# Performance work log

Measured on AMD Instinct MI355X. Metric: run time of the kernel, lower is better.

Reference implementation:

```python
import jax, jax.numpy as jnp
import numpy as np

NOISE_DIM = 128
IN_FEATURES = 512
OUT_FEATURES = 512
BATCH = 256


def setup_inputs() -> dict:
    key = jax.random.key(0)
    k1, k2, k3 = jax.random.split(key, 3)
    out_dim = IN_FEATURES * OUT_FEATURES + OUT_FEATURES
    # x = [noise | features]
    x = jax.random.normal(k1, (BATCH, NOISE_DIM + IN_FEATURES), dtype=jnp.float32)
    # hypermodel Linear params; scale ~ 1/sqrt(fan_in) like torch default init
    scale = 1.0 / np.sqrt(NOISE_DIM)
    W = jax.random.uniform(k2, (NOISE_DIM, out_dim), dtype=jnp.float32, minval=-scale, maxval=scale)
    b = jax.random.uniform(k3, (out_dim,), dtype=jnp.float32, minval=-scale, maxval=scale)
    return {"x": x, "W": W, "b": b}


def reference(x, W, b):
    # split input into hypernet noise and features
    noise = x[:, :NOISE_DIM]            # [B, noise_dim]
    feats = x[:, NOISE_DIM:]            # [B, in_features]
    # hypermodel: generate per-sample linear params
    params = noise @ W + b              # [B, in*out + out]
    w_flat = params[:, : IN_FEATURES * OUT_FEATURES]
    bias = params[:, IN_FEATURES * OUT_FEATURES :]        # [B, out]
    weight = w_flat.reshape(-1, IN_FEATURES, OUT_FEATURES)  # [B, in, out]
    # batched matmul (torch.bmm of [B,1,in] @ [B,in,out]) + bias, squeeze
    out = jnp.einsum("bi,bio->bo", feats, weight) + bias   # [B, out]
    return out
```

## Files before the change

kernel.cpp:

```cpp
#include <hip/hip_runtime.h>
#include <hip/hip_bf16.h>
#include <stdint.h>

namespace {
constexpr int kBatch = 256;
constexpr int kNoise = 128;
constexpr int kIn    = 512;
constexpr int kOut   = 512;
constexpr int kXCols = kNoise + kIn;
constexpr int kPCols = kIn * kOut + kOut;
constexpr int kOTile = 32;
constexpr int kITile = 16;
constexpr int kSplits = kIn / kITile;
constexpr int kWStride = 68;
constexpr int kFeatsStride = 260;
}

typedef __bf16 bf16x8 __attribute__((ext_vector_type(8)));
typedef float  f32x4  __attribute__((ext_vector_type(4)));
typedef unsigned int u32x4 __attribute__((ext_vector_type(4)));

__device__ inline unsigned int pack_bf16x2(float lo, float hi) {
    unsigned int a = (unsigned int)__builtin_bit_cast(unsigned short, (__bf16)lo);
    unsigned int b = (unsigned int)__builtin_bit_cast(unsigned short, (__bf16)hi);
    return a | (b << 16);
}

__device__ inline void wg_barrier_lds() {
    __asm__ volatile("" ::: "memory");
    __builtin_amdgcn_s_waitcnt(0xC07F);
    __builtin_amdgcn_s_barrier();
    __asm__ volatile("" ::: "memory");
}

__global__ __launch_bounds__(512, 4)
void hyper_gemm_kernel(const float* __restrict__ x,
                       const float* __restrict__ W,
                       const float* __restrict__ bvec,
                       float* __restrict__ part)
{
    const int tid  = threadIdx.x;
    const int lane = tid & 63;
    const int wave = tid >> 6;
    const int q    = lane >> 4;
    const int l16  = lane & 15;

    const int o0 = blockIdx.x * kOTile;
    const int i0 = blockIdx.y * kITile;

    const int u    = tid >> 3;
    const int colg = (tid & 7) * 4;

    __shared__ unsigned int wtile[2][kOTile * kWStride];
    __shared__ float feats_lds[kITile * kFeatsStride];
    __shared__ float bv_lds[(kITile + 1) * kOTile];

    const int nPass = (blockIdx.y == 0) ? (kITile + 1) : kITile;

    auto pass_cbase = [&](int p) -> size_t {
        return (p == kITile) ? (size_t)(kIn * kOut) : (size_t)(i0 + p) * kOut;
    };
    auto wrow = [&](int p) -> const float* {
        return W + (size_t)(2 * u) * kPCols + pass_cbase(p) + o0 + colg;
    };

    f32x4 pa0, pa1, pb0, pb1;
    { const float* wp = wrow(0); pa0 = *(const f32x4*)wp; pa1 = *(const f32x4*)(wp + kPCols); }
    { const float* wp = wrow(1); pb0 = *(const f32x4*)wp; pb1 = *(const f32x4*)(wp + kPCols); }

    for (int idx = tid; idx < (kITile + 1) * kOTile; idx += 512) {
        const int p = idx >> 5, c = idx & 31;
        const size_t cb = (p == kITile) ? (size_t)(kIn * kOut) : (size_t)(i0 + p) * kOut;
        bv_lds[idx] = bvec[cb + o0 + c];
    }

    {
        const int i    = tid & 15;
        const int brow = tid >> 4;
        #pragma unroll
        for (int rep = 0; rep < 8; ++rep) {
            const int b = brow + rep * 32;
            feats_lds[i * kFeatsStride + b] = x[b * kXCols + kNoise + i0 + i];
        }
    }

    bf16x8 afrag[2][4];
    {
        #pragma unroll
        for (int mt = 0; mt < 2; ++mt) {
            const float* xr = x + (size_t)(wave * 32 + mt * 16 + l16) * kXCols;
            #pragma unroll
            for (int s = 0; s < 4; ++s) {
                const float* p = xr + s * 32 + q * 8;
                f32x4 u0 = *(const f32x4*)(p);
                f32x4 u1 = *(const f32x4*)(p + 4);
                bf16x8 a;
                a[0] = (__bf16)u0[0]; a[1] = (__bf16)u0[1];
                a[2] = (__bf16)u0[2]; a[3] = (__bf16)u0[3];
                a[4] = (__bf16)u1[0]; a[5] = (__bf16)u1[1];
                a[6] = (__bf16)u1[2]; a[7] = (__bf16)u1[3];
                afrag[mt][s] = a;
            }
        }
    }

    float oacc[2][2][4];
    #pragma unroll
    for (int mt = 0; mt < 2; ++mt)
        #pragma unroll
        for (int nt = 0; nt < 2; ++nt)
            #pragma unroll
            for (int r = 0; r < 4; ++r) oacc[mt][nt][r] = 0.f;

    __syncthreads();

    for (int ip = 0; ip < nPass; ++ip) {
        unsigned int pk[4];
        #pragma unroll
        for (int cc = 0; cc < 4; ++cc) pk[cc] = pack_bf16x2(pa0[cc], pa1[cc]);

        unsigned int* wt = &wtile[ip & 1][0];
        #pragma unroll
        for (int cc = 0; cc < 4; ++cc)
            wt[(colg + cc) * kWStride + u] = pk[cc];

        pa0 = pb0; pa1 = pb1;
        if (ip + 2 < nPass) {
            const float* wp = wrow(ip + 2);
            pb0 = *(const f32x4*)wp; pb1 = *(const f32x4*)(wp + kPCols);
        }

        wg_barrier_lds();

        f32x4 acc[2][2];
        const f32x4 zero = {0.f, 0.f, 0.f, 0.f};
        #pragma unroll
        for (int mt = 0; mt < 2; ++mt)
            #pragma unroll
            for (int nt = 0; nt < 2; ++nt) acc[mt][nt] = zero;

        #pragma unroll
        for (int s = 0; s < 4; ++s) {
            #pragma unroll
            for (int nt = 0; nt < 2; ++nt) {
                u32x4 raw = *(const u32x4*)&wt[(nt * 16 + l16) * kWStride + s * 16 + q * 4];
                bf16x8 bfrag = __builtin_bit_cast(bf16x8, raw);
                #pragma unroll
                for (int mt = 0; mt < 2; ++mt)
                    acc[mt][nt] = __builtin_amdgcn_mfma_f32_16x16x32_bf16(
                        afrag[mt][s], bfrag, acc[mt][nt], 0, 0, 0);
            }
        }

        const float bv0 = bv_lds[ip * kOTile + l16];
        const float bv1 = bv_lds[ip * kOTile + 16 + l16];

        if (ip < kITile) {
            #pragma unroll
            for (int mt = 0; mt < 2; ++mt) {
                const f32x4 f4 = *(const f32x4*)&feats_lds[ip * kFeatsStride
                                        + wave * 32 + mt * 16 + q * 4];
                #pragma unroll
                for (int r = 0; r < 4; ++r) {
                    oacc[mt][0][r] += f4[r] * (acc[mt][0][r] + bv0);
                    oacc[mt][1][r] += f4[r] * (acc[mt][1][r] + bv1);
                }
            }
        } else {
            #pragma unroll
            for (int mt = 0; mt < 2; ++mt)
                #pragma unroll
                for (int r = 0; r < 4; ++r) {
                    oacc[mt][0][r] += acc[mt][0][r] + bv0;
                    oacc[mt][1][r] += acc[mt][1][r] + bv1;
                }
        }
    }

    float* pp = part + (size_t)blockIdx.y * kBatch * kOut;
    #pragma unroll
    for (int mt = 0; mt < 2; ++mt)
        #pragma unroll
        for (int nt = 0; nt < 2; ++nt) {
            const int o = o0 + nt * 16 + l16;
            #pragma unroll
            for (int r = 0; r < 4; ++r) {
                const int b = wave * 32 + mt * 16 + q * 4 + r;
                pp[(size_t)b * kOut + o] = oacc[mt][nt][r];
            }
        }
}

__global__ __launch_bounds__(256)
void reduce_kernel(const float* __restrict__ part, float* __restrict__ out)
{
    const size_t idx4 = ((size_t)blockIdx.x * 256 + threadIdx.x) * 4;
    f32x4 acc = *(const f32x4*)(part + idx4);
    #pragma unroll
    for (int s = 1; s < kSplits; ++s)
        acc += *(const f32x4*)(part + (size_t)s * kBatch * kOut + idx4);
    *(f32x4*)(out + idx4) = acc;
}

extern "C" void kernel_launch(void* const* d_in, const int* in_sizes, int n_in,
                              void* d_out, int out_size, void* d_ws, size_t ws_size,
                              hipStream_t stream) {
    const float* x  = (const float*)d_in[0];
    const float* W  = (const float*)d_in[1];
    const float* bv = (const float*)d_in[2];
    float* out  = (float*)d_out;
    float* part = (float*)d_ws;

    dim3 grid(kOut / kOTile, kSplits);
    hyper_gemm_kernel<<<grid, 512, 0, stream>>>(x, W, bv, part);

    const int n4 = kBatch * kOut / 4;
    reduce_kernel<<<n4 / 256, 256, 0, stream>>>(part, out);
}
```

Measured before the change: 217.6 us.

## Refactor contraction to fold features into noise operand, split noise dim with atomics

The GEMM is reorganized so each pass multiplies (feature times noise) as the A operand against a bf16 tile of W, and the results accumulate directly in MFMA accumulators across input rows. This avoids the separate per-pass epilogue. The noise dimension is split across a third grid axis, with atomicAdd into zeroed partial slabs via a memset. The bias-vector and W-bias contributions become extra MFMA passes, with the final bias added in the reduce. Output tiles widen to 128 columns with a swizzled LDS layout, which adds atomic traffic and a memset launch in exchange for more parallelism and higher MFMA utilization.

```diff
diff --git a/kernel.cpp b/kernel.cpp
--- a/kernel.cpp
+++ b/kernel.cpp
@@ -9,11 +9,13 @@
 constexpr int kOut   = 512;
 constexpr int kXCols = kNoise + kIn;
 constexpr int kPCols = kIn * kOut + kOut;
-constexpr int kOTile = 32;
-constexpr int kITile = 16;
-constexpr int kSplits = kIn / kITile;
-constexpr int kWStride = 68;
+constexpr int kWBias = kIn * kOut;
+constexpr int kOTileC = 128;
+constexpr int kITile  = 16;
+constexpr int kNChunk = 32;
+constexpr int kWTStride = 20;
 constexpr int kFeatsStride = 260;
+constexpr int kSlabs = 32;
 }
 
 typedef __bf16 bf16x8 __attribute__((ext_vector_type(8)));
@@ -32,6 +34,8 @@
     __builtin_amdgcn_s_barrier();
     __asm__ volatile("" ::: "memory");
 }
+
+struct PInfo { const float* p; int stride; int rowlim; };
 
 __global__ __launch_bounds__(512, 4)
 void hyper_gemm_kernel(const float* __restrict__ x,
@@ -45,34 +49,52 @@
     const int q    = lane >> 4;
     const int l16  = lane & 15;
 
-    const int o0 = blockIdx.x * kOTile;
-    const int i0 = blockIdx.y * kITile;
-
-    const int u    = tid >> 3;
-    const int colg = (tid & 7) * 4;
-
-    __shared__ unsigned int wtile[2][kOTile * kWStride];
+    const int obk = blockIdx.x;
+    const int isp = blockIdx.y;
+    const int nc  = blockIdx.z;
+    const int o0  = obk * kOTileC;
+    const int i0  = isp * kITile;
+    const int n0  = nc  * kNChunk;
+
+    const bool hasBv = (nc == 0);
+    const bool hasWb = (isp == 0);
+    const int nPass = kITile + (hasBv ? 1 : 0) + (hasWb ? 1 : 0);
+
+    const int rp = tid >> 5;
+    const int w  = tid & 31;
+    const int wkey = w & 3;
+    const int rkey = (l16 >> 2) & 3;
+
+    __shared__ unsigned int wtile[2][kOTileC * kWTStride];
     __shared__ float feats_lds[kITile * kFeatsStride];
-    __shared__ float bv_lds[(kITile + 1) * kOTile];
-
-    const int nPass = (blockIdx.y == 0) ? (kITile + 1) : kITile;
-
-    auto pass_cbase = [&](int p) -> size_t {
-        return (p == kITile) ? (size_t)(kIn * kOut) : (size_t)(i0 + p) * kOut;
+
+    auto ptype = [&](int p) -> int {
+        if (p < kITile) return 0;
+        if (p == kITile) return hasBv ? 1 : 2;
+        return 2;
     };
-    auto wrow = [&](int p) -> const float* {
-        return W + (size_t)(2 * u) * kPCols + pass_cbase(p) + o0 + colg;
+    auto pinfo = [&](int p) -> PInfo {
+        const int t = ptype(p);
+        if (t == 0) return { W + (size_t)n0 * kPCols + (size_t)(i0 + p) * kOut + o0, kPCols, 32 };
+        if (t == 1) return { bvec + (size_t)i0 * kOut + o0, kOut, kITile };
+        return { W + (size_t)n0 * kPCols + kWBias + o0, kPCols, 32 };
     };
-
-    f32x4 pa0, pa1, pb0, pb1;
-    { const float* wp = wrow(0); pa0 = *(const f32x4*)wp; pa1 = *(const f32x4*)(wp + kPCols); }
-    { const float* wp = wrow(1); pb0 = *(const f32x4*)wp; pb1 = *(const f32x4*)(wp + kPCols); }
-
-    for (int idx = tid; idx < (kITile + 1) * kOTile; idx += 512) {
-        const int p = idx >> 5, c = idx & 31;
-        const size_t cb = (p == kITile) ? (size_t)(kIn * kOut) : (size_t)(i0 + p) * kOut;
-        bv_lds[idx] = bvec[cb + o0 + c];
-    }
+    auto load_pass = [&](int p, f32x4& lo, f32x4& hi) {
+        const PInfo pi = pinfo(p);
+        const int r = 2 * rp;
+        if (r < pi.rowlim) {
+            const float* base = pi.p + (size_t)r * pi.stride + 4 * w;
+            lo = *(const f32x4*)base;
+            hi = *(const f32x4*)(base + pi.stride);
+        } else {
+            lo = f32x4{0.f, 0.f, 0.f, 0.f};
+            hi = f32x4{0.f, 0.f, 0.f, 0.f};
+        }
+    };
+
+    f32x4 pla0, pla1, plb0, plb1;
+    load_pass(0, pla0, pla1);
+    load_pass(1, plb0, plb1);
 
     {
         const int i    = tid & 15;
@@ -80,124 +102,117 @@
         #pragma unroll
         for (int rep = 0; rep < 8; ++rep) {
             const int b = brow + rep * 32;
-            feats_lds[i * kFeatsStride + b] = x[b * kXCols + kNoise + i0 + i];
-        }
-    }
-
-    bf16x8 afrag[2][4];
-    {
-        #pragma unroll
-        for (int mt = 0; mt < 2; ++mt) {
-            const float* xr = x + (size_t)(wave * 32 + mt * 16 + l16) * kXCols;
-            #pragma unroll
-            for (int s = 0; s < 4; ++s) {
-                const float* p = xr + s * 32 + q * 8;
-                f32x4 u0 = *(const f32x4*)(p);
-                f32x4 u1 = *(const f32x4*)(p + 4);
-                bf16x8 a;
-                a[0] = (__bf16)u0[0]; a[1] = (__bf16)u0[1];
-                a[2] = (__bf16)u0[2]; a[3] = (__bf16)u0[3];
-                a[4] = (__bf16)u1[0]; a[5] = (__bf16)u1[1];
-                a[6] = (__bf16)u1[2]; a[7] = (__bf16)u1[3];
-                afrag[mt][s] = a;
-            }
-        }
-    }
-
-    float oacc[2][2][4];
-    #pragma unroll
-    for (int mt = 0; mt < 2; ++mt)
-        #pragma unroll
-        for (int nt = 0; nt < 2; ++nt)
-            #pragma unroll
-            for (int r = 0; r < 4; ++r) oacc[mt][nt][r] = 0.f;
+            feats_lds[i * kFeatsStride + b] = x[(size_t)b * kXCols + kNoise + i0 + i];
+        }
+    }
+
+    f32x4 nz[2][2];
+    #pragma unroll
+    for (int m = 0; m < 2; ++m) {
+        const float* xr = x + (size_t)((wave * 2 + m) * 16 + l16) * kXCols + n0 + q * 8;
+        nz[m][0] = *(const f32x4*)xr;
+        nz[m][1] = *(const f32x4*)(xr + 4);
+    }
+
+    f32x4 oacc[2][8];
+    #pragma unroll
+    for (int m = 0; m < 2; ++m)
+        #pragma unroll
+        for (int fo = 0; fo < 8; ++fo) oacc[m][fo] = f32x4{0.f, 0.f, 0.f, 0.f};
 
     __syncthreads();
 
     for (int ip = 0; ip < nPass; ++ip) {
         unsigned int pk[4];
         #pragma unroll
-        for (int cc = 0; cc < 4; ++cc) pk[cc] = pack_bf16x2(pa0[cc], pa1[cc]);
+        for (int cc = 0; cc < 4; ++cc) pk[cc] = pack_bf16x2(pla0[cc], pla1[cc]);
 
         unsigned int* wt = &wtile[ip & 1][0];
         #pragma unroll
         for (int cc = 0; cc < 4; ++cc)
-            wt[(colg + cc) * kWStride + u] = pk[cc];
-
-        pa0 = pb0; pa1 = pb1;
-        if (ip + 2 < nPass) {
-            const float* wp = wrow(ip + 2);
-            pb0 = *(const f32x4*)wp; pb1 = *(const f32x4*)(wp + kPCols);
-        }
+            wt[(4 * w + cc) * kWTStride + ((((rp >> 2) ^ wkey) << 2) | (rp & 3))] = pk[cc];
+
+        pla0 = plb0; pla1 = plb1;
+        if (ip + 2 < nPass) load_pass(ip + 2, plb0, plb1);
 
         wg_barrier_lds();
 
-        f32x4 acc[2][2];
-        const f32x4 zero = {0.f, 0.f, 0.f, 0.f};
-        #pragma unroll
-        for (int mt = 0; mt < 2; ++mt)
-            #pragma unroll
-            for (int nt = 0; nt < 2; ++nt) acc[mt][nt] = zero;
-
-        #pragma unroll
-        for (int s = 0; s < 4; ++s) {
-            #pragma unroll
-            for (int nt = 0; nt < 2; ++nt) {
-                u32x4 raw = *(const u32x4*)&wt[(nt * 16 + l16) * kWStride + s * 16 + q * 4];
-                bf16x8 bfrag = __builtin_bit_cast(bf16x8, raw);
+        const int t = ptype(ip);
+        bf16x8 afr[2];
+        if (t == 0) {
+            #pragma unroll
+            for (int m = 0; m < 2; ++m) {
+                const float f = feats_lds[ip * kFeatsStride + (wave * 2 + m) * 16 + l16];
+                bf16x8 a;
                 #pragma unroll
-                for (int mt = 0; mt < 2; ++mt)
-                    acc[mt][nt] = __builtin_amdgcn_mfma_f32_16x16x32_bf16(
-                        afrag[mt][s], bfrag, acc[mt][nt], 0, 0, 0);
+                for (int j = 0; j < 4; ++j) {
+                    a[j]     = (__bf16)(f * nz[m][0][j]);
+                    a[j + 4] = (__bf16)(f * nz[m][1][j]);
+                }
+                afr[m] = a;
             }
-        }
-
-        const float bv0 = bv_lds[ip * kOTile + l16];
-        const float bv1 = bv_lds[ip * kOTile + 16 + l16];
-
-        if (ip < kITile) {
-            #pragma unroll
-            for (int mt = 0; mt < 2; ++mt) {
-                const f32x4 f4 = *(const f32x4*)&feats_lds[ip * kFeatsStride
-                                        + wave * 32 + mt * 16 + q * 4];
+        } else if (t == 2) {
+            #pragma unroll
+            for (int m = 0; m < 2; ++m) {
+                bf16x8 a;
                 #pragma unroll
-                for (int r = 0; r < 4; ++r) {
-                    oacc[mt][0][r] += f4[r] * (acc[mt][0][r] + bv0);
-                    oacc[mt][1][r] += f4[r] * (acc[mt][1][r] + bv1);
+                for (int j = 0; j < 4; ++j) {
+                    a[j]     = (__bf16)nz[m][0][j];
+                    a[j + 4] = (__bf16)nz[m][1][j];
                 }
+                afr[m] = a;
             }
         } else {
             #pragma unroll
-            for (int mt = 0; mt < 2; ++mt)
+            for (int m = 0; m < 2; ++m) {
+                const int b = (wave * 2 + m) * 16 + l16;
+                bf16x8 a;
                 #pragma unroll
-                for (int r = 0; r < 4; ++r) {
-                    oacc[mt][0][r] += acc[mt][0][r] + bv0;
-                    oacc[mt][1][r] += acc[mt][1][r] + bv1;
+                for (int j = 0; j < 8; ++j) {
+                    const int kk = q * 8 + j;
+                    const float v = feats_lds[(kk & 15) * kFeatsStride + b];
+                    a[j] = (kk < kITile) ? (__bf16)v : (__bf16)0.f;
                 }
-        }
-    }
-
-    float* pp = part + (size_t)blockIdx.y * kBatch * kOut;
-    #pragma unroll
-    for (int mt = 0; mt < 2; ++mt)
-        #pragma unroll
-        for (int nt = 0; nt < 2; ++nt) {
-            const int o = o0 + nt * 16 + l16;
-            #pragma unroll
-            for (int r = 0; r < 4; ++r) {
-                const int b = wave * 32 + mt * 16 + q * 4 + r;
-                pp[(size_t)b * kOut + o] = oacc[mt][nt][r];
+                afr[m] = a;
             }
         }
+
+        #pragma unroll
+        for (int fo = 0; fo < 8; ++fo) {
+            const int col = fo * 16 + l16;
+            u32x4 raw = *(const u32x4*)&wt[col * kWTStride + ((q ^ rkey) << 2)];
+            bf16x8 bfr = __builtin_bit_cast(bf16x8, raw);
+            #pragma unroll
+            for (int m = 0; m < 2; ++m)
+                oacc[m][fo] = __builtin_amdgcn_mfma_f32_16x16x32_bf16(
+                    afr[m], bfr, oacc[m][fo], 0, 0, 0);
+        }
+    }
+
+    float* pp = part + (size_t)isp * (kBatch * kOut);
+    #pragma unroll
+    for (int m = 0; m < 2; ++m) {
+        const int bb = (wave * 2 + m) * 16 + q * 4;
+        #pragma unroll
+        for (int fo = 0; fo < 8; ++fo) {
+            const int o = o0 + fo * 16 + l16;
+            #pragma unroll
+            for (int r = 0; r < 4; ++r)
+                atomicAdd(&pp[(size_t)(bb + r) * kOut + o], oacc[m][fo][r]);
+        }
+    }
 }
 
 __global__ __launch_bounds__(256)
-void reduce_kernel(const float* __restrict__ part, float* __restrict__ out)
+void reduce_kernel(const float* __restrict__ part,
+                   const float* __restrict__ bvec,
+                   float* __restrict__ out)
 {
     const size_t idx4 = ((size_t)blockIdx.x * 256 + threadIdx.x) * 4;
-    f32x4 acc = *(const f32x4*)(part + idx4);
-    #pragma unroll
-    for (int s = 1; s < kSplits; ++s)
+    const int o = (int)(idx4 & (kOut - 1));
+    f32x4 acc = *(const f32x4*)(bvec + kWBias + o);
+    #pragma unroll
+    for (int s = 0; s < kSlabs; ++s)
         acc += *(const f32x4*)(part + (size_t)s * kBatch * kOut + idx4);
     *(f32x4*)(out + idx4) = acc;
 }
@@ -211,9 +226,11 @@
     float* out  = (float*)d_out;
     float* part = (float*)d_ws;
 
-    dim3 grid(kOut / kOTile, kSplits);
+    hipMemsetAsync(part, 0, (size_t)kSlabs * kBatch * kOut * sizeof(float), stream);
+
+    dim3 grid(kOut / kOTileC, kIn / kITile, kNoise / kNChunk);
     hyper_gemm_kernel<<<grid, 512, 0, stream>>>(x, W, bv, part);
 
     const int n4 = kBatch * kOut / 4;
-    reduce_kernel<<<n4 / 256, 256, 0, stream>>>(part, out);
-}
+    reduce_kernel<<<n4 / 256, 256, 0, stream>>>(part, bv, out);
+}
```

Result: slower. 261.2 us (+20.1%).

## Restructure W loads to per-column scalar gathers with register ring and peeled bias pass

Applied to the files above, without the earlier changes.

Each thread now loads one output column across 8 consecutive noise rows as scalar loads (coalesced 32-wide per row) instead of 4-wide vectors over 2 rows, then packs them into a single 128-bit LDS store. The main loop is fully unrolled over the fixed 16 passes, and the bias-generating pass for split 0 is peeled out of the loop, with its weights preloaded up front. Occupancy hint drops from 4 to 2 blocks to allow more registers for the unrolled loop and ring buffer. This targets the per-pass branching and the strided LDS transpose writes, at the cost of more global load instructions and possibly lower occupancy.

```diff
diff --git a/kernel.cpp b/kernel.cpp
--- a/kernel.cpp
+++ b/kernel.cpp
@@ -9,11 +9,13 @@
 constexpr int kOut   = 512;
 constexpr int kXCols = kNoise + kIn;
 constexpr int kPCols = kIn * kOut + kOut;
+constexpr int kWBias = kIn * kOut;
 constexpr int kOTile = 32;
 constexpr int kITile = 16;
 constexpr int kSplits = kIn / kITile;
 constexpr int kWStride = 68;
 constexpr int kFeatsStride = 260;
+constexpr int kDepth = 2;
 }
 
 typedef __bf16 bf16x8 __attribute__((ext_vector_type(8)));
@@ -33,7 +35,7 @@
     __asm__ volatile("" ::: "memory");
 }
 
-__global__ __launch_bounds__(512, 4)
+__global__ __launch_bounds__(512, 2)
 void hyper_gemm_kernel(const float* __restrict__ x,
                        const float* __restrict__ W,
                        const float* __restrict__ bvec,
@@ -48,29 +50,40 @@
     const int o0 = blockIdx.x * kOTile;
     const int i0 = blockIdx.y * kITile;
 
-    const int u    = tid >> 3;
-    const int colg = (tid & 7) * 4;
+    const int col = tid & 31;
+    const int kpp = tid >> 5;
 
     __shared__ unsigned int wtile[2][kOTile * kWStride];
     __shared__ float feats_lds[kITile * kFeatsStride];
     __shared__ float bv_lds[(kITile + 1) * kOTile];
 
-    const int nPass = (blockIdx.y == 0) ? (kITile + 1) : kITile;
-
-    auto pass_cbase = [&](int p) -> size_t {
-        return (p == kITile) ? (size_t)(kIn * kOut) : (size_t)(i0 + p) * kOut;
+    const bool hasWb = (blockIdx.y == 0);
+
+    auto wbase = [&](int p) -> const float* {
+        return W + (size_t)(8 * kpp) * kPCols + (size_t)(i0 + p) * kOut + o0 + col;
     };
-    auto wrow = [&](int p) -> const float* {
-        return W + (size_t)(2 * u) * kPCols + pass_cbase(p) + o0 + colg;
-    };
-
-    f32x4 pa0, pa1, pb0, pb1;
-    { const float* wp = wrow(0); pa0 = *(const f32x4*)wp; pa1 = *(const f32x4*)(wp + kPCols); }
-    { const float* wp = wrow(1); pb0 = *(const f32x4*)wp; pb1 = *(const f32x4*)(wp + kPCols); }
+
+    float wb[8];
+    #pragma unroll
+    for (int e = 0; e < 8; ++e) wb[e] = 0.f;
+    if (hasWb) {
+        const float* bp = W + (size_t)(8 * kpp) * kPCols + kWBias + o0 + col;
+        #pragma unroll
+        for (int e = 0; e < 8; ++e) wb[e] = bp[(size_t)e * kPCols];
+    }
+
+    float ring[kDepth][8];
+    #pragma unroll
+    for (int p = 0; p < kDepth; ++p) {
+        const float* wp = wbase(p);
+        #pragma unroll
+        for (int e = 0; e < 8; ++e)
+            ring[p][e] = wp[(size_t)e * kPCols];
+    }
 
     for (int idx = tid; idx < (kITile + 1) * kOTile; idx += 512) {
         const int p = idx >> 5, c = idx & 31;
-        const size_t cb = (p == kITile) ? (size_t)(kIn * kOut) : (size_t)(i0 + p) * kOut;
+        const size_t cb = (p == kITile) ? (size_t)kWBias : (size_t)(i0 + p) * kOut;
         bv_lds[idx] = bvec[cb + o0 + c];
     }
 
@@ -80,27 +93,25 @@
         #pragma unroll
         for (int rep = 0; rep < 8; ++rep) {
             const int b = brow + rep * 32;
-            feats_lds[i * kFeatsStride + b] = x[b * kXCols + kNoise + i0 + i];
+            feats_lds[i * kFeatsStride + b] = x[(size_t)b * kXCols + kNoise + i0 + i];
         }
     }
 
     bf16x8 afrag[2][4];
-    {
-        #pragma unroll
-        for (int mt = 0; mt < 2; ++mt) {
-            const float* xr = x + (size_t)(wave * 32 + mt * 16 + l16) * kXCols;
-            #pragma unroll
-            for (int s = 0; s < 4; ++s) {
-                const float* p = xr + s * 32 + q * 8;
-                f32x4 u0 = *(const f32x4*)(p);
-                f32x4 u1 = *(const f32x4*)(p + 4);
-                bf16x8 a;
-                a[0] = (__bf16)u0[0]; a[1] = (__bf16)u0[1];
-                a[2] = (__bf16)u0[2]; a[3] = (__bf16)u0[3];
-                a[4] = (__bf16)u1[0]; a[5] = (__bf16)u1[1];
-                a[6] = (__bf16)u1[2]; a[7] = (__bf16)u1[3];
-                afrag[mt][s] = a;
-            }
+    #pragma unroll
+    for (int mt = 0; mt < 2; ++mt) {
+        const float* xr = x + (size_t)(wave * 32 + mt * 16 + l16) * kXCols;
+        #pragma unroll
+        for (int s = 0; s < 4; ++s) {
+            const float* p = xr + s * 32 + q * 8;
+            f32x4 u0 = *(const f32x4*)(p);
+            f32x4 u1 = *(const f32x4*)(p + 4);
+            bf16x8 a;
+            a[0] = (__bf16)u0[0]; a[1] = (__bf16)u0[1];
+            a[2] = (__bf16)u0[2]; a[3] = (__bf16)u0[3];
+            a[4] = (__bf16)u1[0]; a[5] = (__bf16)u1[1];
+            a[6] = (__bf16)u1[2]; a[7] = (__bf16)u1[3];
+            afrag[mt][s] = a;
         }
     }
 
@@ -114,67 +125,104 @@
 
     __syncthreads();
 
-    for (int ip = 0; ip < nPass; ++ip) {
-        unsigned int pk[4];
-        #pragma unroll
-        for (int cc = 0; cc < 4; ++cc) pk[cc] = pack_bf16x2(pa0[cc], pa1[cc]);
+    #pragma unroll
+    for (int ip = 0; ip < kITile; ++ip) {
+        const int slot = ip & (kDepth - 1);
+
+        u32x4 pk;
+        pk[0] = pack_bf16x2(ring[slot][0], ring[slot][1]);
+        pk[1] = pack_bf16x2(ring[slot][2], ring[slot][3]);
+        pk[2] = pack_bf16x2(ring[slot][4], ring[slot][5]);
+        pk[3] = pack_bf16x2(ring[slot][6], ring[slot][7]);
 
         unsigned int* wt = &wtile[ip & 1][0];
-        #pragma unroll
-        for (int cc = 0; cc < 4; ++cc)
-            wt[(colg + cc) * kWStride + u] = pk[cc];
-
-        pa0 = pb0; pa1 = pb1;
-        if (ip + 2 < nPass) {
-            const float* wp = wrow(ip + 2);
-            pb0 = *(const f32x4*)wp; pb1 = *(const f32x4*)(wp + kPCols);
+        *(u32x4*)&wt[col * kWStride + 4 * kpp] = pk;
+
+        if (ip + kDepth < kITile) {
+            const float* wp = wbase(ip + kDepth);
+            #pragma unroll
+            for (int e = 0; e < 8; ++e)
+                ring[slot][e] = wp[(size_t)e * kPCols];
         }
 
         wg_barrier_lds();
 
         f32x4 acc[2][2];
-        const f32x4 zero = {0.f, 0.f, 0.f, 0.f};
         #pragma unroll
         for (int mt = 0; mt < 2; ++mt)
             #pragma unroll
-            for (int nt = 0; nt < 2; ++nt) acc[mt][nt] = zero;
+            for (int nt = 0; nt < 2; ++nt) acc[mt][nt] = f32x4{0.f, 0.f, 0.f, 0.f};
 
         #pragma unroll
         for (int s = 0; s < 4; ++s) {
+            bf16x8 bfr[2];
             #pragma unroll
             for (int nt = 0; nt < 2; ++nt) {
                 u32x4 raw = *(const u32x4*)&wt[(nt * 16 + l16) * kWStride + s * 16 + q * 4];
-                bf16x8 bfrag = __builtin_bit_cast(bf16x8, raw);
+                bfr[nt] = __builtin_bit_cast(bf16x8, raw);
+            }
+            #pragma unroll
+            for (int mt = 0; mt < 2; ++mt)
                 #pragma unroll
-                for (int mt = 0; mt < 2; ++mt)
+                for (int nt = 0; nt < 2; ++nt)
                     acc[mt][nt] = __builtin_amdgcn_mfma_f32_16x16x32_bf16(
-                        afrag[mt][s], bfrag, acc[mt][nt], 0, 0, 0);
-            }
+                        afrag[mt][s], bfr[nt], acc[mt][nt], 0, 0, 0);
         }
 
         const float bv0 = bv_lds[ip * kOTile + l16];
         const float bv1 = bv_lds[ip * kOTile + 16 + l16];
-
-        if (ip < kITile) {
-            #pragma unroll
-            for (int mt = 0; mt < 2; ++mt) {
-                const f32x4 f4 = *(const f32x4*)&feats_lds[ip * kFeatsStride
-                                        + wave * 32 + mt * 16 + q * 4];
-                #pragma unroll
-                for (int r = 0; r < 4; ++r) {
-                    oacc[mt][0][r] += f4[r] * (acc[mt][0][r] + bv0);
-                    oacc[mt][1][r] += f4[r] * (acc[mt][1][r] + bv1);
-                }
-            }
-        } else {
+        #pragma unroll
+        for (int mt = 0; mt < 2; ++mt) {
+            const f32x4 f4 = *(const f32x4*)&feats_lds[ip * kFeatsStride
+                                    + wave * 32 + mt * 16 + q * 4];
+            #pragma unroll
+            for (int r = 0; r < 4; ++r) {
+                oacc[mt][0][r] += f4[r] * (acc[mt][0][r] + bv0);
+                oacc[mt][1][r] += f4[r] * (acc[mt][1][r] + bv1);
+            }
+        }
+    }
+
+    if (hasWb) {
+        u32x4 pk;
+        pk[0] = pack_bf16x2(wb[0], wb[1]);
+        pk[1] = pack_bf16x2(wb[2], wb[3]);
+        pk[2] = pack_bf16x2(wb[4], wb[5]);
+        pk[3] = pack_bf16x2(wb[6], wb[7]);
+        unsigned int* wt = &wtile[0][0];
+        *(u32x4*)&wt[col * kWStride + 4 * kpp] = pk;
+        wg_barrier_lds();
+
+        f32x4 acc[2][2];
+        #pragma unroll
+        for (int mt = 0; mt < 2; ++mt)
+            #pragma unroll
+            for (int nt = 0; nt < 2; ++nt) acc[mt][nt] = f32x4{0.f, 0.f, 0.f, 0.f};
+
+        #pragma unroll
+        for (int s = 0; s < 4; ++s) {
+            bf16x8 bfr[2];
+            #pragma unroll
+            for (int nt = 0; nt < 2; ++nt) {
+                u32x4 raw = *(const u32x4*)&wt[(nt * 16 + l16) * kWStride + s * 16 + q * 4];
+                bfr[nt] = __builtin_bit_cast(bf16x8, raw);
+            }
             #pragma unroll
             for (int mt = 0; mt < 2; ++mt)
                 #pragma unroll
-                for (int r = 0; r < 4; ++r) {
-                    oacc[mt][0][r] += acc[mt][0][r] + bv0;
-                    oacc[mt][1][r] += acc[mt][1][r] + bv1;
-                }
-        }
+                for (int nt = 0; nt < 2; ++nt)
+                    acc[mt][nt] = __builtin_amdgcn_mfma_f32_16x16x32_bf16(
+                        afrag[mt][s], bfr[nt], acc[mt][nt], 0, 0, 0);
+        }
+        const float bv0 = bv_lds[kITile * kOTile + l16];
+        const float bv1 = bv_lds[kITile * kOTile + 16 + l16];
+        #pragma unroll
+        for (int mt = 0; mt < 2; ++mt)
+            #pragma unroll
+            for (int r = 0; r < 4; ++r) {
+                oacc[mt][0][r] += acc[mt][0][r] + bv0;
+                oacc[mt][1][r] += acc[mt][1][r] + bv1;
+            }
     }
 
     float* pp = part + (size_t)blockIdx.y * kBatch * kOut;
```

After: 241.9 us. 1.11x slower.
